# Optimization experiments

Measured on AMD Instinct MI355X. Metric: run time of the kernel, lower is better.

The kernel has to match this reference:

```python
import jax, jax.numpy as jnp
import numpy as np

DIM = 768
NUM_HEADS = 12
HEAD_DIM = DIM // NUM_HEADS
SCALE = HEAD_DIM ** (-0.5)
LN_EPS = 1e-5


def setup_inputs() -> dict:
    key = jax.random.key(0)
    ks = jax.random.split(key, 8)
    B, K, C = 4, 2048, DIM
    return {
        "x": jax.random.normal(ks[0], (B, K, C), jnp.float32),
        "pos_embed": jax.random.normal(ks[1], (B, K, C), jnp.float32),
        "rel_pos_bias": jax.random.normal(ks[2], (B, K, K), jnp.float32),
        "ln_g": jnp.ones((C,), jnp.float32),
        "ln_b": jnp.zeros((C,), jnp.float32),
        "qkv_w": jax.random.normal(ks[3], (C, 3 * C), jnp.float32) * 0.02,
        "qkv_b": jnp.zeros((3 * C,), jnp.float32),
        "proj_w": jax.random.normal(ks[4], (C, C), jnp.float32) * 0.02,
        "proj_b": jnp.zeros((C,), jnp.float32),
    }


def _layernorm(x, g, b):
    mu = jnp.mean(x, axis=-1, keepdims=True)
    var = jnp.mean(jnp.square(x - mu), axis=-1, keepdims=True)
    return (x - mu) * jax.lax.rsqrt(var + LN_EPS) * g + b


def reference(x, pos_embed, rel_pos_bias, ln_g, ln_b, qkv_w, qkv_b, proj_w, proj_b):
    B, K, C = x.shape
    H, D = NUM_HEADS, HEAD_DIM
    xp = _layernorm(x, ln_g, ln_b) + pos_embed
    qkv = xp @ qkv_w + qkv_b                      # [B,K,3C]
    qkv = qkv.reshape(B, K, 3, H, D)
    q = jnp.transpose(qkv[:, :, 0], (0, 2, 1, 3))  # [B,H,K,D]
    k = jnp.transpose(qkv[:, :, 1], (0, 2, 1, 3))
    v = jnp.transpose(qkv[:, :, 2], (0, 2, 1, 3))
    attn = jnp.einsum("bhqd,bhkd->bhqk", q, k) * SCALE
    attn = attn + rel_pos_bias[:, None, :, :]
    attn = jax.nn.softmax(attn, axis=-1)
    out = jnp.einsum("bhqk,bhkd->bhqd", attn, v)   # [B,H,K,D]
    out = jnp.transpose(out, (0, 2, 1, 3)).reshape(B, K, C)
    # DropPath(0.1) is identity in eval mode
    return out @ proj_w + proj_b
```

## Files before the change

kernel.cpp:

```cpp
#include <hip/hip_runtime.h>
#include <hip/hip_bf16.h>
#include <stdint.h>

typedef __attribute__((ext_vector_type(4))) float f32x4;
typedef __attribute__((ext_vector_type(16))) float f32x16;
typedef __attribute__((ext_vector_type(8))) short s16x8;
typedef __attribute__((ext_vector_type(4))) short s16x4;
typedef uint16_t u16;

#define DEV __device__ __forceinline__

static DEV u16 f2bf(float f) {
  union { float f; uint32_t u; } v; v.f = f;
  uint32_t r = v.u + 0x7fffu + ((v.u >> 16) & 1u);
  return (u16)(r >> 16);
}

static DEV float bf2f(u16 x) {
  union { uint32_t u; float f; } v; v.u = ((uint32_t)x) << 16;
  return v.f;
}

static DEV uint32_t cvt_pk_bf16(float lo, float hi) {
  uint32_t r;
  asm("v_cvt_pk_bf16_f32 %0, %1, %2" : "=v"(r) : "v"(lo), "v"(hi));
  return r;
}

#define GLD_LDS16(gp, lp) __builtin_amdgcn_global_load_lds( \
    (const __attribute__((address_space(1))) void*)(gp),    \
    (__attribute__((address_space(3))) void*)(lp), 16, 0, 0)

__global__ __launch_bounds__(256) void k_bcast(
    const float* __restrict__ in, u16* __restrict__ out) {
  size_t i = ((size_t)blockIdx.x * 256 + threadIdx.x) * 8;
  f32x4 a = *(const f32x4*)(in + i);
  f32x4 b = *(const f32x4*)(in + i + 4);
  s16x8 o;
#pragma unroll
  for (int j = 0; j < 4; ++j) o[j] = (short)f2bf(a[j] * 1.4426950409f);
#pragma unroll
  for (int j = 0; j < 4; ++j) o[4 + j] = (short)f2bf(b[j] * 1.4426950409f);
  *(s16x8*)(out + i) = o;
}

__global__ __launch_bounds__(256) void k_ln(
    const float* __restrict__ x, const float* __restrict__ pos,
    const float* __restrict__ g, const float* __restrict__ be,
    u16* __restrict__ xp) {
  int row = blockIdx.x;
  size_t base = (size_t)row * 768;
  int t = threadIdx.x;
  float v0 = x[base + t], v1 = x[base + t + 256], v2 = x[base + t + 512];
  float s = v0 + v1 + v2;
  float ss = v0 * v0 + v1 * v1 + v2 * v2;
#pragma unroll
  for (int off = 1; off < 64; off <<= 1) {
    s += __shfl_xor(s, off);
    ss += __shfl_xor(ss, off);
  }
  __shared__ float red[8];
  int wave = t >> 6, lane = t & 63;
  if (lane == 0) { red[wave] = s; red[4 + wave] = ss; }
  __syncthreads();
  float tot = red[0] + red[1] + red[2] + red[3];
  float tss = red[4] + red[5] + red[6] + red[7];
  float mu = tot * (1.0f / 768.0f);
  float var = tss * (1.0f / 768.0f) - mu * mu;
  float rs = rsqrtf(var + 1e-5f);
  float vv[3] = {v0, v1, v2};
#pragma unroll
  for (int i = 0; i < 3; ++i) {
    int c = t + i * 256;
    float val = (vv[i] - mu) * rs * g[c] + be[c] + pos[base + c];
    xp[base + c] = f2bf(val);
  }
}

__global__ __launch_bounds__(256) void k_tr(
    const float* __restrict__ in, u16* __restrict__ out, int K, int N) {
  __shared__ float tile[32][33];
  int n0 = blockIdx.x * 32, k0 = blockIdx.y * 32;
  int tx = threadIdx.x & 31, ty = threadIdx.x >> 5;
#pragma unroll
  for (int r = ty; r < 32; r += 8)
    tile[r][tx] = in[(size_t)(k0 + r) * N + n0 + tx];
  __syncthreads();
#pragma unroll
  for (int r = ty; r < 32; r += 8)
    out[(size_t)(n0 + r) * K + k0 + tx] = f2bf(tile[tx][r]);
}

__global__ __launch_bounds__(256) void k_gemm_qkv(
    const u16* __restrict__ A, const u16* __restrict__ Bt,
    const float* __restrict__ bias, u16* __restrict__ qkv,
    u16* __restrict__ vtg) {
  __shared__ u16 Al[128 * 64];
  __shared__ u16 Bl[128 * 64];
  const size_t BHKD = (size_t)48 * 2048 * 64;
  int mt = blockIdx.x, nt = blockIdx.y;
  int t = threadIdx.x, wave = t >> 6, lane = t & 63;
  int lr = lane & 15, lg = lane >> 4;
  f32x4 acc[4][4];
#pragma unroll
  for (int i = 0; i < 4; ++i)
#pragma unroll
    for (int j = 0; j < 4; ++j) acc[i][j] = (f32x4){0.f, 0.f, 0.f, 0.f};
  const size_t Ab = (size_t)mt * 128 * 768;
  const size_t Bb = (size_t)nt * 128 * 768;
  int wr = (wave >> 1) * 64, wc = (wave & 1) * 64;
  for (int kt = 0; kt < 12; ++kt) {
#pragma unroll
    for (int c = 0; c < 4; ++c) {
      int q = c * 256 + t;
      int row = q >> 3, ch = q & 7;
      int sc = ch ^ (row & 7);
      GLD_LDS16(A + Ab + (size_t)row * 768 + kt * 64 + sc * 8,
                &Al[(size_t)(c * 256 + wave * 64) * 8]);
      GLD_LDS16(Bt + Bb + (size_t)row * 768 + kt * 64 + sc * 8,
                &Bl[(size_t)(c * 256 + wave * 64) * 8]);
    }
    __syncthreads();
#pragma unroll
    for (int ki = 0; ki < 2; ++ki) {
      s16x8 af[4], bf[4];
#pragma unroll
      for (int mi = 0; mi < 4; ++mi)
        af[mi] = *(const s16x8*)&Al[(wr + mi * 16 + lr) * 64 +
                                    (((ki * 4 + lg) ^ (lr & 7)) * 8)];
#pragma unroll
      for (int ni = 0; ni < 4; ++ni)
        bf[ni] = *(const s16x8*)&Bl[(wc + ni * 16 + lr) * 64 +
                                    (((ki * 4 + lg) ^ (lr & 7)) * 8)];
#pragma unroll
      for (int mi = 0; mi < 4; ++mi)
#pragma unroll
        for (int ni = 0; ni < 4; ++ni)
          acc[mi][ni] = __builtin_amdgcn_mfma_f32_16x16x32_bf16(
              af[mi], bf[ni], acc[mi][ni], 0, 0, 0);
    }
    __syncthreads();
  }
  int which0 = (nt * 128) / 768;
  float qscale = (which0 == 0) ? 0.1803368801f : 1.0f;
#pragma unroll
  for (int ni = 0; ni < 4; ++ni) {
    int col = wc + ni * 16 + lr;
    int n = nt * 128 + col;
    int which = n / 768, cc = n % 768;
    int h = cc >> 6, d = cc & 63;
    float bs = bias[n];
    if (which == 2) {
#pragma unroll
      for (int mi = 0; mi < 4; ++mi) {
        int m0 = mt * 128 + wr + mi * 16 + lg * 4;
        int b = m0 >> 11, kp0 = m0 & 2047;
        s16x4 o4;
#pragma unroll
        for (int j = 0; j < 4; ++j) o4[j] = (short)f2bf(acc[mi][ni][j] + bs);
        *(s16x4*)&vtg[((size_t)(b * 12 + h) * 64 + d) * 2048 + kp0] = o4;
      }
    } else {
#pragma unroll
      for (int mi = 0; mi < 4; ++mi) {
#pragma unroll
        for (int j = 0; j < 4; ++j) {
          int row = wr + mi * 16 + lg * 4 + j;
          int m = mt * 128 + row;
          int b = m >> 11, kp = m & 2047;
          size_t dst = (size_t)which * BHKD +
                       (((size_t)b * 12 + h) * 2048 + kp) * 64 + d;
          qkv[dst] = f2bf((acc[mi][ni][j] + bs) * qscale);
        }
      }
    }
  }
}

#define STAGE_KV(KB, VB, ktt) do {                                          \
  _Pragma("unroll")                                                         \
  for (int c_ = 0; c_ < 2; ++c_) {                                          \
    int q_ = c_ * 256 + t; int r_ = q_ >> 3, ch_ = q_ & 7;                  \
    int sc_ = ch_ ^ (r_ & 7);                                               \
    int gk_ = (r_ & 0x33) | ((r_ & 4) << 1) | ((r_ & 8) >> 1);              \
    GLD_LDS16(Kg + ((size_t)((ktt) * 64 + gk_)) * 64 + sc_ * 8,             \
              &KB[(c_ * 256 + wave * 64) * 8]);                             \
    GLD_LDS16(Vt + (size_t)r_ * 2048 + (ktt) * 64 + sc_ * 8,                \
              &VB[(c_ * 256 + wave * 64) * 8]);                             \
  }                                                                         \
} while (0)

#define LOAD_B(BR, ktt) do {                                                \
  const u16* bp_ = Bgl + (ktt) * 64;                                        \
  BR[0] = *(const s16x8*)(bp_);                                             \
  BR[1] = *(const s16x8*)(bp_ + 16);                                        \
  BR[2] = *(const s16x8*)(bp_ + 32);                                        \
  BR[3] = *(const s16x8*)(bp_ + 48);                                        \
} while (0)

#define COMPUTE_TILE(KB, VB, BV) do {                                       \
  f32x16 sa_[2];                                                            \
  _Pragma("unroll")                                                         \
  for (int kv_ = 0; kv_ < 2; ++kv_)                                         \
    _Pragma("unroll")                                                       \
    for (int r = 0; r < 16; ++r)                                            \
      sa_[kv_][r] = bf2f((u16)BV[kv_ * 2 + (r >> 3)][r & 7]);               \
  __builtin_amdgcn_s_setprio(1);                                            \
  _Pragma("unroll")                                                         \
  for (int ki = 0; ki < 4; ++ki) {                                          \
    _Pragma("unroll")                                                       \
    for (int kv_ = 0; kv_ < 2; ++kv_) {                                     \
      s16x8 kf = *(const s16x8*)&KB[(kv_ * 32 + l31) * 64 +                 \
                                    (((ki * 2 + hi) ^ (l31 & 7)) * 8)];     \
      sa_[kv_] = __builtin_amdgcn_mfma_f32_32x32x16_bf16(kf, qf[ki],        \
                                                         sa_[kv_], 0, 0, 0);\
    }                                                                       \
  }                                                                         \
  __builtin_amdgcn_s_setprio(0);                                            \
  float p_[32];                                                             \
  _Pragma("unroll")                                                         \
  for (int kv_ = 0; kv_ < 2; ++kv_)                                         \
    _Pragma("unroll")                                                       \
    for (int r = 0; r < 16; ++r)                                            \
      p_[kv_ * 16 + r] = exp2f(sa_[kv_][r]);                                \
  float tm_[16];                                                            \
  _Pragma("unroll")                                                         \
  for (int i = 0; i < 16; ++i) tm_[i] = p_[i] + p_[i + 16];                 \
  _Pragma("unroll")                                                         \
  for (int off = 8; off >= 1; off >>= 1)                                    \
    _Pragma("unroll")                                                       \
    for (int i = 0; i < off; ++i) tm_[i] += tm_[i + off];                   \
  l_run += tm_[0];                                                          \
  union { uint32_t u[4]; s16x8 v; } pa_[4];                                 \
  _Pragma("unroll")                                                         \
  for (int s = 0; s < 4; ++s)                                               \
    _Pragma("unroll")                                                       \
    for (int w = 0; w < 4; ++w)                                             \
      pa_[s].u[w] = cvt_pk_bf16(p_[(s >> 1) * 16 + (s & 1) * 8 + 2 * w],    \
                                p_[(s >> 1) * 16 + (s & 1) * 8 + 2 * w + 1]);\
  __builtin_amdgcn_s_setprio(1);                                            \
  _Pragma("unroll")                                                         \
  for (int s = 0; s < 4; ++s) {                                             \
    _Pragma("unroll")                                                       \
    for (int dt = 0; dt < 2; ++dt) {                                        \
      s16x8 vf = *(const s16x8*)&VB[(dt * 32 + l31) * 64 +                  \
                                    (((s * 2 + hi) ^ (l31 & 7)) * 8)];      \
      oacc[dt] = __builtin_amdgcn_mfma_f32_32x32x16_bf16(vf, pa_[s].v,      \
                                                         oacc[dt], 0, 0, 0);\
    }                                                                       \
  }                                                                         \
  __builtin_amdgcn_s_setprio(0);                                            \
} while (0)

__global__ __launch_bounds__(256, 3) void k_attn(
    const u16* __restrict__ qkv, const u16* __restrict__ vtg,
    const u16* __restrict__ biasb, u16* __restrict__ ctx) {
  __shared__ u16 Kl[3][64 * 64];
  __shared__ u16 Vl[3][64 * 64];
  int bid = blockIdx.x;
  int swz = (bid & 7) * 96 + (bid >> 3);
  int h = swz % 12;
  int bq = swz / 12;
  int qt = bq & 15;
  int b = bq >> 4;
  int bh = b * 12 + h;
  int t = threadIdx.x, wave = t >> 6, lane = t & 63;
  int l31 = lane & 31, hi = lane >> 5;
  const size_t BHKD = (size_t)48 * 2048 * 64;
  const u16* Q = qkv + (size_t)bh * 2048 * 64;
  const u16* Kg = Q + BHKD;
  const u16* Vt = vtg + (size_t)bh * 64 * 2048;
  int qrow = qt * 128 + wave * 32 + l31;
  const u16* Bgl = biasb + ((size_t)b * 2048 + qrow) * 2048 + hi * 8;
  s16x8 qf[4];
#pragma unroll
  for (int ki = 0; ki < 4; ++ki)
    qf[ki] = *(const s16x8*)&Q[(size_t)qrow * 64 + ki * 16 + hi * 8];
  f32x16 oacc[2];
#pragma unroll
  for (int r = 0; r < 16; ++r) { oacc[0][r] = 0.f; oacc[1][r] = 0.f; }
  float l_run = 0.f;

  STAGE_KV(Kl[0], Vl[0], 0);
  STAGE_KV(Kl[1], Vl[1], 1);
  asm volatile("s_waitcnt vmcnt(4)" ::: "memory");
  __builtin_amdgcn_s_barrier();
  __builtin_amdgcn_sched_barrier(0);

  int cur = 0;
#pragma unroll 1
  for (int kt = 0; kt < 32; ++kt) {
    s16x8 bv_[4];
    LOAD_B(bv_, kt);
    int nb = cur + 2; if (nb >= 3) nb -= 3;
    if (kt + 2 < 32) STAGE_KV(Kl[nb], Vl[nb], kt + 2);
    COMPUTE_TILE(Kl[cur], Vl[cur], bv_);
    asm volatile("s_waitcnt vmcnt(4)" ::: "memory");
    __builtin_amdgcn_sched_barrier(0);
    __builtin_amdgcn_s_barrier();
    __builtin_amdgcn_sched_barrier(0);
    cur = cur + 1; if (cur >= 3) cur = 0;
  }
  float l_tot = l_run + __shfl_xor(l_run, 32);
  float inv = 1.0f / l_tot;
  size_t obase = ((size_t)b * 2048 + qrow) * 768 + h * 64;
#pragma unroll
  for (int dt = 0; dt < 2; ++dt) {
#pragma unroll
    for (int g = 0; g < 4; ++g) {
      s16x4 o4;
#pragma unroll
      for (int j = 0; j < 4; ++j)
        o4[j] = (short)f2bf(oacc[dt][g * 4 + j] * inv);
      *(s16x4*)&ctx[obase + dt * 32 + g * 8 + hi * 4] = o4;
    }
  }
}

__global__ __launch_bounds__(256) void k_gemm_proj(
    const u16* __restrict__ A, const u16* __restrict__ Bt,
    const float* __restrict__ bias, float* __restrict__ out) {
  __shared__ u16 Al[128 * 64];
  __shared__ u16 Bl[128 * 64];
  int mt = blockIdx.x, nt = blockIdx.y;
  int t = threadIdx.x, wave = t >> 6, lane = t & 63;
  int lr = lane & 15, lg = lane >> 4;
  f32x4 acc[4][4];
#pragma unroll
  for (int i = 0; i < 4; ++i)
#pragma unroll
    for (int j = 0; j < 4; ++j) acc[i][j] = (f32x4){0.f, 0.f, 0.f, 0.f};
  const size_t Ab = (size_t)mt * 128 * 768;
  const size_t Bb = (size_t)nt * 128 * 768;
  int wr = (wave >> 1) * 64, wc = (wave & 1) * 64;
  for (int kt = 0; kt < 12; ++kt) {
#pragma unroll
    for (int c = 0; c < 4; ++c) {
      int q = c * 256 + t;
      int row = q >> 3, ch = q & 7;
      int sc = ch ^ (row & 7);
      GLD_LDS16(A + Ab + (size_t)row * 768 + kt * 64 + sc * 8,
                &Al[(size_t)(c * 256 + wave * 64) * 8]);
      GLD_LDS16(Bt + Bb + (size_t)row * 768 + kt * 64 + sc * 8,
                &Bl[(size_t)(c * 256 + wave * 64) * 8]);
    }
    __syncthreads();
#pragma unroll
    for (int ki = 0; ki < 2; ++ki) {
      s16x8 af[4], bf[4];
#pragma unroll
      for (int mi = 0; mi < 4; ++mi)
        af[mi] = *(const s16x8*)&Al[(wr + mi * 16 + lr) * 64 +
                                    (((ki * 4 + lg) ^ (lr & 7)) * 8)];
#pragma unroll
      for (int ni = 0; ni < 4; ++ni)
        bf[ni] = *(const s16x8*)&Bl[(wc + ni * 16 + lr) * 64 +
                                    (((ki * 4 + lg) ^ (lr & 7)) * 8)];
#pragma unroll
      for (int mi = 0; mi < 4; ++mi)
#pragma unroll
        for (int ni = 0; ni < 4; ++ni)
          acc[mi][ni] = __builtin_amdgcn_mfma_f32_16x16x32_bf16(
              af[mi], bf[ni], acc[mi][ni], 0, 0, 0);
    }
    __syncthreads();
  }
#pragma unroll
  for (int ni = 0; ni < 4; ++ni) {
    int col = wc + ni * 16 + lr;
    int n = nt * 128 + col;
    float bs = bias[n];
#pragma unroll
    for (int mi = 0; mi < 4; ++mi) {
#pragma unroll
      for (int j = 0; j < 4; ++j) {
        int row = wr + mi * 16 + lg * 4 + j;
        out[(size_t)(mt * 128 + row) * 768 + n] = acc[mi][ni][j] + bs;
      }
    }
  }
}

extern "C" void kernel_launch(void* const* d_in, const int* in_sizes, int n_in,
                              void* d_out, int out_size, void* d_ws, size_t ws_size,
                              hipStream_t stream) {
  const float* x      = (const float*)d_in[0];
  const float* pos    = (const float*)d_in[1];
  const float* bias   = (const float*)d_in[2];
  const float* ln_g   = (const float*)d_in[3];
  const float* ln_b   = (const float*)d_in[4];
  const float* qkv_w  = (const float*)d_in[5];
  const float* qkv_b  = (const float*)d_in[6];
  const float* proj_w = (const float*)d_in[7];
  const float* proj_b = (const float*)d_in[8];
  float* out = (float*)d_out;

  char* ws = (char*)d_ws;
  u16* xp      = (u16*)ws;              ws += 12582912;
  u16* qkv_wt  = (u16*)ws;              ws += 3538944;
  u16* proj_wt = (u16*)ws;              ws += 1179648;
  u16* qkvbuf  = (u16*)ws;              ws += 25165824;
  u16* ctx     = (u16*)ws;              ws += 12582912;
  u16* vtg     = (u16*)ws;              ws += 12582912;
  u16* biasb   = (u16*)ws;              ws += 33554432;

  k_bcast<<<8192, 256, 0, stream>>>(bias, biasb);
  k_ln<<<8192, 256, 0, stream>>>(x, pos, ln_g, ln_b, xp);
  k_tr<<<dim3(72, 24), 256, 0, stream>>>(qkv_w, qkv_wt, 768, 2304);
  k_tr<<<dim3(24, 24), 256, 0, stream>>>(proj_w, proj_wt, 768, 768);
  k_gemm_qkv<<<dim3(64, 18), 256, 0, stream>>>(xp, qkv_wt, qkv_b, qkvbuf, vtg);
  k_attn<<<768, 256, 0, stream>>>(qkvbuf, vtg, biasb, ctx);
  k_gemm_proj<<<dim3(64, 6), 256, 0, stream>>>(ctx, proj_wt, proj_b, out);
}
```

Before: 200.8 us.

## Fold bias conversion into QKV GEMM, compute row sums via MFMA

Removes the standalone bias-conversion kernel and has each QKV GEMM block first convert a grid-strided slice of rel_pos_bias to scaled bf16, which saves one launch. The attention kernel drops its scalar per-row reduction of softmax probabilities and instead accumulates row sums with an extra MFMA against a vector of bf16 ones. Occupancy hint for attention drops from 3 to 2 waves-groups per CU to make room for the extra accumulator registers. The GEMM prologue now carries a large memory-bound copy, and the row sums are built from bf16-rounded probabilities.

```diff
diff --git a/kernel.cpp b/kernel.cpp
--- a/kernel.cpp
+++ b/kernel.cpp
@@ -30,19 +30,6 @@
 #define GLD_LDS16(gp, lp) __builtin_amdgcn_global_load_lds( \
     (const __attribute__((address_space(1))) void*)(gp),    \
     (__attribute__((address_space(3))) void*)(lp), 16, 0, 0)
-
-__global__ __launch_bounds__(256) void k_bcast(
-    const float* __restrict__ in, u16* __restrict__ out) {
-  size_t i = ((size_t)blockIdx.x * 256 + threadIdx.x) * 8;
-  f32x4 a = *(const f32x4*)(in + i);
-  f32x4 b = *(const f32x4*)(in + i + 4);
-  s16x8 o;
-#pragma unroll
-  for (int j = 0; j < 4; ++j) o[j] = (short)f2bf(a[j] * 1.4426950409f);
-#pragma unroll
-  for (int j = 0; j < 4; ++j) o[4 + j] = (short)f2bf(b[j] * 1.4426950409f);
-  *(s16x8*)(out + i) = o;
-}
 
 __global__ __launch_bounds__(256) void k_ln(
     const float* __restrict__ x, const float* __restrict__ pos,
@@ -94,13 +81,29 @@
 __global__ __launch_bounds__(256) void k_gemm_qkv(
     const u16* __restrict__ A, const u16* __restrict__ Bt,
     const float* __restrict__ bias, u16* __restrict__ qkv,
-    u16* __restrict__ vtg) {
+    u16* __restrict__ vtg, const float* __restrict__ biasf,
+    u16* __restrict__ biasb) {
   __shared__ u16 Al[128 * 64];
   __shared__ u16 Bl[128 * 64];
   const size_t BHKD = (size_t)48 * 2048 * 64;
   int mt = blockIdx.x, nt = blockIdx.y;
   int t = threadIdx.x, wave = t >> 6, lane = t & 63;
   int lr = lane & 15, lg = lane >> 4;
+  {
+    size_t tid = ((size_t)(nt * 64 + mt) * 256 + t) * 8;
+    size_t stride = (size_t)1152 * 256 * 8;
+    const size_t NB = (size_t)4 * 2048 * 2048;
+    for (size_t i = tid; i < NB; i += stride) {
+      f32x4 a = *(const f32x4*)(biasf + i);
+      f32x4 b = *(const f32x4*)(biasf + i + 4);
+      s16x8 o;
+#pragma unroll
+      for (int j = 0; j < 4; ++j) o[j] = (short)f2bf(a[j] * 1.4426950409f);
+#pragma unroll
+      for (int j = 0; j < 4; ++j) o[4 + j] = (short)f2bf(b[j] * 1.4426950409f);
+      *(s16x8*)(biasb + i) = o;
+    }
+  }
   f32x4 acc[4][4];
 #pragma unroll
   for (int i = 0; i < 4; ++i)
@@ -223,14 +226,6 @@
     _Pragma("unroll")                                                       \
     for (int r = 0; r < 16; ++r)                                            \
       p_[kv_ * 16 + r] = exp2f(sa_[kv_][r]);                                \
-  float tm_[16];                                                            \
-  _Pragma("unroll")                                                         \
-  for (int i = 0; i < 16; ++i) tm_[i] = p_[i] + p_[i + 16];                 \
-  _Pragma("unroll")                                                         \
-  for (int off = 8; off >= 1; off >>= 1)                                    \
-    _Pragma("unroll")                                                       \
-    for (int i = 0; i < off; ++i) tm_[i] += tm_[i + off];                   \
-  l_run += tm_[0];                                                          \
   union { uint32_t u[4]; s16x8 v; } pa_[4];                                 \
   _Pragma("unroll")                                                         \
   for (int s = 0; s < 4; ++s)                                               \
@@ -241,6 +236,8 @@
   __builtin_amdgcn_s_setprio(1);                                            \
   _Pragma("unroll")                                                         \
   for (int s = 0; s < 4; ++s) {                                             \
+    lacc = __builtin_amdgcn_mfma_f32_32x32x16_bf16(onesv, pa_[s].v,         \
+                                                   lacc, 0, 0, 0);          \
     _Pragma("unroll")                                                       \
     for (int dt = 0; dt < 2; ++dt) {                                        \
       s16x8 vf = *(const s16x8*)&VB[(dt * 32 + l31) * 64 +                  \
@@ -252,7 +249,7 @@
   __builtin_amdgcn_s_setprio(0);                                            \
 } while (0)
 
-__global__ __launch_bounds__(256, 3) void k_attn(
+__global__ __launch_bounds__(256, 2) void k_attn(
     const u16* __restrict__ qkv, const u16* __restrict__ vtg,
     const u16* __restrict__ biasb, u16* __restrict__ ctx) {
   __shared__ u16 Kl[3][64 * 64];
@@ -276,10 +273,12 @@
 #pragma unroll
   for (int ki = 0; ki < 4; ++ki)
     qf[ki] = *(const s16x8*)&Q[(size_t)qrow * 64 + ki * 16 + hi * 8];
-  f32x16 oacc[2];
-#pragma unroll
-  for (int r = 0; r < 16; ++r) { oacc[0][r] = 0.f; oacc[1][r] = 0.f; }
-  float l_run = 0.f;
+  s16x8 onesv;
+#pragma unroll
+  for (int i = 0; i < 8; ++i) onesv[i] = (short)0x3F80;
+  f32x16 oacc[2], lacc;
+#pragma unroll
+  for (int r = 0; r < 16; ++r) { oacc[0][r] = 0.f; oacc[1][r] = 0.f; lacc[r] = 0.f; }
 
   STAGE_KV(Kl[0], Vl[0], 0);
   STAGE_KV(Kl[1], Vl[1], 1);
@@ -301,8 +300,7 @@
     __builtin_amdgcn_sched_barrier(0);
     cur = cur + 1; if (cur >= 3) cur = 0;
   }
-  float l_tot = l_run + __shfl_xor(l_run, 32);
-  float inv = 1.0f / l_tot;
+  float inv = 1.0f / lacc[0];
   size_t obase = ((size_t)b * 2048 + qrow) * 768 + h * 64;
 #pragma unroll
   for (int dt = 0; dt < 2; ++dt) {
@@ -404,11 +402,11 @@
   u16* vtg     = (u16*)ws;              ws += 12582912;
   u16* biasb   = (u16*)ws;              ws += 33554432;
 
-  k_bcast<<<8192, 256, 0, stream>>>(bias, biasb);
   k_ln<<<8192, 256, 0, stream>>>(x, pos, ln_g, ln_b, xp);
   k_tr<<<dim3(72, 24), 256, 0, stream>>>(qkv_w, qkv_wt, 768, 2304);
   k_tr<<<dim3(24, 24), 256, 0, stream>>>(proj_w, proj_wt, 768, 768);
-  k_gemm_qkv<<<dim3(64, 18), 256, 0, stream>>>(xp, qkv_wt, qkv_b, qkvbuf, vtg);
+  k_gemm_qkv<<<dim3(64, 18), 256, 0, stream>>>(xp, qkv_wt, qkv_b, qkvbuf, vtg,
+                                               bias, biasb);
   k_attn<<<768, 256, 0, stream>>>(qkvbuf, vtg, biasb, ctx);
   k_gemm_proj<<<dim3(64, 6), 256, 0, stream>>>(ctx, proj_wt, proj_b, out);
 }
```

Measured after the change: 200.6 us. About the same (-0.1%).
